# Optimization experiments

Hardware: AMD Instinct MI355X
Metric: run time of the kernel (lower is better)

## Reference

```python
import jax, jax.numpy as jnp
import numpy as np

N_PROBLEMS = 20000
N_SKILLS = 1000
EMB_SIZE = 128
TIME_LOG = 5.0
B, L = 64, 1024


def setup_inputs() -> dict:
    key = jax.random.key(0)
    ks = jax.random.split(key, 10)
    skills = jax.random.randint(ks[0], (B, L), 0, N_SKILLS)
    problems = jax.random.randint(ks[1], (B, L), 0, N_PROBLEMS)
    labels = jax.random.randint(ks[2], (B, L), 0, 2)
    times = jnp.sort(jax.random.randint(ks[3], (B, L), 0, 1_000_000), axis=-1)
    inp = jnp.stack([skills, problems, labels, times], axis=1)  # [B,4,L]
    std = 0.01
    return {
        "input": inp,
        "problem_base": std * jax.random.normal(ks[4], (N_PROBLEMS, 1), jnp.float32),
        "skill_base": std * jax.random.normal(ks[5], (N_SKILLS, 1), jnp.float32),
        "alpha_inter": std * jax.random.normal(ks[6], (N_SKILLS * 2, EMB_SIZE), jnp.float32),
        "alpha_skill": std * jax.random.normal(ks[7], (N_SKILLS, EMB_SIZE), jnp.float32),
        "beta_inter": std * jax.random.normal(ks[8], (N_SKILLS * 2, EMB_SIZE), jnp.float32),
        "beta_skill": std * jax.random.normal(ks[9], (N_SKILLS, EMB_SIZE), jnp.float32),
    }


def reference(input, problem_base, skill_base, alpha_inter, alpha_skill, beta_inter, beta_skill):
    skills = input[:, 0]    # [B,L]
    problems = input[:, 1]
    labels = input[:, 2]
    times = input[:, 3]

    mask_labels = labels * (labels < 2).astype(labels.dtype)
    inters = skills + mask_labels * N_SKILLS  # [B,L] in [0, 2*N_SKILLS)

    # pairwise Hawkes excitation / decay scores: [B,L,L]
    alphas = jnp.einsum('bie,bje->bij', alpha_inter[inters], alpha_skill[skills])
    betas = jnp.einsum('bie,bje->bij', beta_inter[inters], beta_skill[skills])
    betas = jnp.clip(betas + 1.0, 0.0, 10.0)

    dt = jnp.abs(times[:, :, None] - times[:, None, :]).astype(jnp.float32)
    log_dt = jnp.log(dt + 1e-10) / np.log(TIME_LOG)

    cross_effects = alphas * jnp.exp(-betas * log_dt)

    seq_len = skills.shape[1]
    # keep strictly-upper-triangular entries (source i before target j)
    keep = jnp.triu(jnp.ones((seq_len, seq_len), dtype=bool), k=1)
    sum_t = jnp.where(keep[None], cross_effects, 0.0).sum(axis=-2)  # [B,L]

    problem_bias = problem_base[problems][..., 0]
    skill_bias = skill_base[skills][..., 0]
    return jax.nn.sigmoid(problem_bias + skill_bias + sum_t)
```

## Files before the change

### kernel.cpp

```cpp
#include <hip/hip_runtime.h>
#include <hip/hip_bf16.h>

#define NB   64
#define SL   1024
#define EMB  128
#define NSK  1000
#define TI   64
#define NS   2

#define AI_OFF 0
#define BI_OFF 256000
#define AS_OFF 512000
#define BS_OFF 640000
#define TB_ELEMS 768000
#define ACC_BYTE_OFF (TB_ELEMS * 2)

#define AI_B 0
#define BI_B 512000
#define AS_B 1024000
#define BS_B 1280000

using short8  = __attribute__((ext_vector_type(8))) short;
using floatx4 = __attribute__((ext_vector_type(4))) float;

#define INV_LOG2_5 0.43067655807339306f

__device__ inline unsigned cvt2(float x, float y) {
    float2 f; f.x = x; f.y = y;
    __hip_bfloat162 h = __float22bfloat162_rn(f);
    unsigned u; __builtin_memcpy(&u, &h, sizeof(u));
    return u;
}

extern "C" __global__ __launch_bounds__(256)
void cvt_tables(const float* __restrict__ ai, const float* __restrict__ bi,
                const float* __restrict__ as, const float* __restrict__ bs,
                unsigned short* __restrict__ dst)
{
    const int t = blockIdx.x * 256 + threadIdx.x;
    const long e = (long)t * 8;
    const float* src;
    if      (e < 256000) src = ai + e;
    else if (e < 512000) src = bi + (e - 256000);
    else if (e < 640000) src = as + (e - 512000);
    else                 src = bs + (e - 640000);
    float4 f0 = *(const float4*)src;
    float4 f1 = *(const float4*)(src + 4);
    uint4 pk;
    pk.x = cvt2(f0.x, f0.y); pk.y = cvt2(f0.z, f0.w);
    pk.z = cvt2(f1.x, f1.y); pk.w = cvt2(f1.z, f1.w);
    *(uint4*)(dst + e) = pk;
}

__device__ float fixup_pair(const float* __restrict__ air,
                            const float* __restrict__ bir,
                            const float* __restrict__ asr,
                            const float* __restrict__ bsr) {
    float da = 0.f, db = 0.f;
#pragma unroll 8
    for (int k = 0; k < EMB; k += 4) {
        float4 a  = *(const float4*)(air + k);
        float4 s  = *(const float4*)(asr + k);
        float4 bq = *(const float4*)(bir + k);
        float4 tt = *(const float4*)(bsr + k);
        da += a.x * s.x + a.y * s.y + a.z * s.z + a.w * s.w;
        db += bq.x * tt.x + bq.y * tt.y + bq.z * tt.z + bq.w * tt.w;
    }
    float beta = fminf(fmaxf(db + 1.f, 0.f), 10.f);
    return da * __expf(beta * 14.30676558073393f);
}

extern "C" __global__ __launch_bounds__(256, 2)
void hawkes_main(const int*   __restrict__ inp,
                 const unsigned short* __restrict__ tb,
                 float*       __restrict__ acc)
{
    __shared__ uint4 ldsq[2048];
    char* ldsc = (char*)ldsq;

    const int bid  = blockIdx.x;
    const int b    = bid & (NB - 1);
    const int r    = bid >> 6;
    const int jt   = 15 - (r >> 1);
    const int s    = r & 1;
    const int tid  = threadIdx.x;
    const int w    = tid >> 6;
    const int l    = tid & 63;
    const int quad = l >> 4;
    const int col  = l & 15;
    const int wrow = w * 16;

    const int* __restrict__ binp = inp + b * 4 * SL;
    const char* __restrict__ tbc = (const char*)tb;

    const int jbase = jt * TI;

    int tjv[4];
#pragma unroll
    for (int strip = 0; strip < 4; ++strip)
        tjv[strip] = binp[3 * SL + jbase + strip * 16 + col];

    {
        const int row  = tid >> 2;
        const int sq   = tid & 3;
        const int skj  = binp[jbase + row];
        const char* srcA = tbc + AS_B + (long)skj * 256 + sq * 64;
        const char* srcB = tbc + BS_B + (long)skj * 256 + sq * 64;
        uint4 qa[4], qb[4];
#pragma unroll
        for (int u = 0; u < 4; ++u) {
            qa[u] = *(const uint4*)(srcA + u * 16);
            qb[u] = *(const uint4*)(srcB + u * 16);
        }
        const int rx = (row & 15) << 4;
        const int wb = row * 256;
#pragma unroll
        for (int u = 0; u < 4; ++u) {
            const int slot = (((4 * sq + u) << 4) ^ rx);
            *(uint4*)(ldsc + wb + slot)         = qa[u];
            *(uint4*)(ldsc + 16384 + wb + slot) = qb[u];
        }
    }
    __syncthreads();

    short8 bfa[4][4], bfb[4][4];
#pragma unroll
    for (int strip = 0; strip < 4; ++strip) {
        const int row   = strip * 16 + col;
        const int rbase = row * 256;
        const int rx    = (row & 15) << 4;
#pragma unroll
        for (int ks = 0; ks < 4; ++ks) {
            const int cb = ((quad + ks * 4) << 4) ^ rx;
            bfa[strip][ks] = *(const short8*)(ldsc + rbase + cb);
            bfb[strip][ks] = *(const short8*)(ldsc + 16384 + rbase + cb);
        }
    }

    int intrv[8];
#pragma unroll
    for (int tt = 0; tt < 8; ++tt) {
        const int arow = (s + 2 * tt) * TI + wrow + col;
        intrv[tt] = binp[arow] + binp[2 * SL + arow] * NSK;
    }

    float sum[4] = {0.f, 0.f, 0.f, 0.f};

#pragma unroll 1
    for (int it = s; it <= jt; it += NS) {
        const int tt = (it - s) >> 1;
        const long ab = (long)intrv[tt] * 256 + quad * 16;
        const char* pA = tbc + AI_B + ab;
        const char* pB = tbc + BI_B + ab;
        short8 av[4], bv[4];
#pragma unroll
        for (int ks = 0; ks < 4; ++ks) {
            av[ks] = *(const short8*)(pA + ks * 64);
            bv[ks] = *(const short8*)(pB + ks * 64);
        }
        const int4 t4 = *(const int4*)(binp + 3 * SL + it * TI + wrow + quad * 4);

        floatx4 aa[4], bb[4];
#pragma unroll
        for (int strip = 0; strip < 4; ++strip) {
            aa[strip] = floatx4{0.f, 0.f, 0.f, 0.f};
            bb[strip] = floatx4{1.f, 1.f, 1.f, 1.f};
        }
#pragma unroll
        for (int ks = 0; ks < 4; ++ks) {
#pragma unroll
            for (int strip = 0; strip < 4; ++strip) {
                aa[strip] = __builtin_amdgcn_mfma_f32_16x16x32_bf16(av[ks], bfa[strip][ks], aa[strip], 0, 0, 0);
                bb[strip] = __builtin_amdgcn_mfma_f32_16x16x32_bf16(bv[ks], bfb[strip][ks], bb[strip], 0, 0, 0);
            }
        }

#pragma unroll
        for (int strip = 0; strip < 4; ++strip) {
            const int tjs = tjv[strip];
#pragma unroll
            for (int rr = 0; rr < 4; ++rr) {
                const int ti = (rr == 0) ? t4.x : (rr == 1) ? t4.y : (rr == 2) ? t4.z : t4.w;
                const int dt = tjs - ti;
                float lc  = __log2f((float)dt);
                float nb  = fminf(fmaxf(bb[strip][rr], 0.f), 10.f) * (-INV_LOG2_5);
                float arg = (dt > 0) ? nb * lc : -__builtin_inff();
                sum[strip] += aa[strip][rr] * __builtin_amdgcn_exp2f(arg);
            }
        }
    }

#pragma unroll
    for (int strip = 0; strip < 4; ++strip) {
        sum[strip] += __shfl_xor(sum[strip], 16, 64);
        sum[strip] += __shfl_xor(sum[strip], 32, 64);
    }
    __syncthreads();
    float* red = (float*)ldsc;
    red[w * 64 + quad * 16 + col] = sum[quad];
    __syncthreads();
    if (w == 0) {
        const float tot = red[l] + red[64 + l] + red[128 + l] + red[192 + l];
        acc[(((long)s * NB + b) << 10) + jbase + l] = tot;
    }
}

extern "C" __global__ __launch_bounds__(256)
void hawkes_finalize(const int* __restrict__ inp, const float* __restrict__ pbase,
                     const float* __restrict__ sbase,
                     const float* __restrict__ ai, const float* __restrict__ as,
                     const float* __restrict__ bi, const float* __restrict__ bs,
                     const float* __restrict__ acc, float* __restrict__ out)
{
    const int t = blockIdx.x * 256 + threadIdx.x;
    const int b = t >> 10, j = t & (SL - 1);
    const int* binp = inp + b * 4 * SL;
    const int tj   = binp[3 * SL + j];
    const int sk_j = binp[j];

    float corr = 0.f;
    for (int i = j - 1; i >= 0 && binp[3 * SL + i] == tj; --i) {
        const int ski = binp[i], li = binp[2 * SL + i];
        const long intr = ski + (long)li * NSK;
        corr += fixup_pair(ai + intr * EMB, bi + intr * EMB,
                           as + (long)sk_j * EMB, bs + (long)sk_j * EMB);
    }

    float sum = acc[t] + acc[NB * SL + t] + corr;
    const float x = pbase[binp[SL + j]] + sbase[sk_j] + sum;
    out[t] = 1.f / (1.f + __expf(-x));
}

extern "C" void kernel_launch(void* const* d_in, const int* in_sizes, int n_in,
                              void* d_out, int out_size, void* d_ws, size_t ws_size,
                              hipStream_t stream) {
    const int*   inp = (const int*)d_in[0];
    const float* pb  = (const float*)d_in[1];
    const float* sb  = (const float*)d_in[2];
    const float* ai  = (const float*)d_in[3];
    const float* as  = (const float*)d_in[4];
    const float* bi  = (const float*)d_in[5];
    const float* bs  = (const float*)d_in[6];

    unsigned short* tb  = (unsigned short*)d_ws;
    float*          acc = (float*)((char*)d_ws + ACC_BYTE_OFF);

    cvt_tables<<<dim3(96000 / 256), dim3(256), 0, stream>>>(ai, bi, as, bs, tb);
    hawkes_main<<<dim3(NB * 16 * NS), dim3(256), 0, stream>>>(inp, tb, acc);
    hawkes_finalize<<<dim3(NB * SL / 256), dim3(256), 0, stream>>>(
        inp, pb, sb, ai, as, bi, bs, acc, (float*)d_out);
}
```

Measured before the change: 119.2 us.

## Stage A-operand rows through double-buffered LDS with register prefetch

Before this change, each wave gathered its alpha/beta interaction rows directly from global memory with strided per-lane loads inside the loop. Now each thread loads contiguous 64-byte chunks of the next-next tile into registers and writes them into a swizzled, double-buffered LDS region while the current tile is computed. MFMA A operands are then read from LDS. This hides gather latency and coalesces global loads. The cost is doubled LDS (64 KB per block, which may limit occupancy to 2 blocks per CU), more registers for the prefetch stage, and a block-wide barrier each iteration.

New measurement: 116.4 us. 1.02x faster.

```diff
diff --git a/kernel.cpp b/kernel.cpp
--- a/kernel.cpp
+++ b/kernel.cpp
@@ -8,10 +8,6 @@
 #define TI   64
 #define NS   2
 
-#define AI_OFF 0
-#define BI_OFF 256000
-#define AS_OFF 512000
-#define BS_OFF 640000
 #define TB_ELEMS 768000
 #define ACC_BYTE_OFF (TB_ELEMS * 2)
 
@@ -70,12 +66,39 @@
     return da * __expf(beta * 14.30676558073393f);
 }
 
+struct Stage2 { uint4 a0, a1, a2, a3, b0, b1, b2, b3; };
+
+__device__ __forceinline__ Stage2 stage_load2(const char* __restrict__ tbc,
+                                              int intr, int sq)
+{
+    const long ab = (long)intr * 256 + sq * 64;
+    const char* pA = tbc + AI_B + ab;
+    const char* pB = tbc + BI_B + ab;
+    Stage2 s;
+    s.a0 = *(const uint4*)(pA);      s.a1 = *(const uint4*)(pA + 16);
+    s.a2 = *(const uint4*)(pA + 32); s.a3 = *(const uint4*)(pA + 48);
+    s.b0 = *(const uint4*)(pB);      s.b1 = *(const uint4*)(pB + 16);
+    s.b2 = *(const uint4*)(pB + 32); s.b3 = *(const uint4*)(pB + 48);
+    return s;
+}
+
+__device__ __forceinline__ void stage_write2(char* buf, int srow, int wslot,
+                                             const Stage2& s)
+{
+    char* pA = buf + srow * 256 + wslot;
+    char* pAx = buf + srow * 256 + (wslot ^ 16);
+    *(uint4*)(pA)        = s.a0;  *(uint4*)(pA + 128)  = s.a1;
+    *(uint4*)(pAx)       = s.a2;  *(uint4*)(pAx + 128) = s.a3;
+    *(uint4*)(pA + 16384)  = s.b0;  *(uint4*)(pA + 16384 + 128)  = s.b1;
+    *(uint4*)(pAx + 16384) = s.b2;  *(uint4*)(pAx + 16384 + 128) = s.b3;
+}
+
 extern "C" __global__ __launch_bounds__(256, 2)
 void hawkes_main(const int*   __restrict__ inp,
                  const unsigned short* __restrict__ tb,
                  float*       __restrict__ acc)
 {
-    __shared__ uint4 ldsq[2048];
+    __shared__ uint4 ldsq[4096];
     char* ldsc = (char*)ldsq;
 
     const int bid  = blockIdx.x;
@@ -92,7 +115,6 @@
 
     const int* __restrict__ binp = inp + b * 4 * SL;
     const char* __restrict__ tbc = (const char*)tb;
-
     const int jbase = jt * TI;
 
     int tjv[4];
@@ -137,55 +159,78 @@
         }
     }
 
+    const int srow  = tid >> 2;
+    const int sq    = tid & 3;
+    const int wslot = (((2 * sq) ^ (srow & 7)) << 4);
     int intrv[8];
 #pragma unroll
     for (int tt = 0; tt < 8; ++tt) {
-        const int arow = (s + 2 * tt) * TI + wrow + col;
+        const int arow = (s + 2 * tt) * TI + srow;
         intrv[tt] = binp[arow] + binp[2 * SL + arow] * NSK;
     }
 
+    int roff[4];
+    {
+        const int qh = quad >> 1, ql = quad & 1, c7 = col & 7;
+#pragma unroll
+        for (int ks = 0; ks < 4; ++ks)
+            roff[ks] = (wrow + col) * 256 + ql * 128 + (((2 * ks + qh) ^ c7) << 4);
+    }
+
     float sum[4] = {0.f, 0.f, 0.f, 0.f};
 
+    if (s <= jt) {
+        const int nt = ((jt - s) >> 1) + 1;
+
+        Stage2 rS = stage_load2(tbc, intrv[0], sq);
+        __syncthreads();
+        stage_write2(ldsc, srow, wslot, rS);
+        if (nt > 1) rS = stage_load2(tbc, intrv[1], sq);
+
 #pragma unroll 1
-    for (int it = s; it <= jt; it += NS) {
-        const int tt = (it - s) >> 1;
-        const long ab = (long)intrv[tt] * 256 + quad * 16;
-        const char* pA = tbc + AI_B + ab;
-        const char* pB = tbc + BI_B + ab;
-        short8 av[4], bv[4];
-#pragma unroll
-        for (int ks = 0; ks < 4; ++ks) {
-            av[ks] = *(const short8*)(pA + ks * 64);
-            bv[ks] = *(const short8*)(pB + ks * 64);
-        }
-        const int4 t4 = *(const int4*)(binp + 3 * SL + it * TI + wrow + quad * 4);
-
-        floatx4 aa[4], bb[4];
-#pragma unroll
-        for (int strip = 0; strip < 4; ++strip) {
-            aa[strip] = floatx4{0.f, 0.f, 0.f, 0.f};
-            bb[strip] = floatx4{1.f, 1.f, 1.f, 1.f};
-        }
-#pragma unroll
-        for (int ks = 0; ks < 4; ++ks) {
+        for (int t = 0; t < nt; ++t) {
+            __syncthreads();
+            const int cur = (t & 1) << 15;
+            if (t + 1 < nt) stage_write2(ldsc + (cur ^ 32768), srow, wslot, rS);
+            if (t + 2 < nt) rS = stage_load2(tbc, intrv[t + 2], sq);
+
+            const int it = s + 2 * t;
+            const char* bufA = ldsc + cur;
+            short8 av[4], bv[4];
+#pragma unroll
+            for (int ks = 0; ks < 4; ++ks) {
+                av[ks] = *(const short8*)(bufA + roff[ks]);
+                bv[ks] = *(const short8*)(bufA + 16384 + roff[ks]);
+            }
+            const int4 t4 = *(const int4*)(binp + 3 * SL + it * TI + wrow + quad * 4);
+
+            floatx4 aa[4], bb[4];
 #pragma unroll
             for (int strip = 0; strip < 4; ++strip) {
-                aa[strip] = __builtin_amdgcn_mfma_f32_16x16x32_bf16(av[ks], bfa[strip][ks], aa[strip], 0, 0, 0);
-                bb[strip] = __builtin_amdgcn_mfma_f32_16x16x32_bf16(bv[ks], bfb[strip][ks], bb[strip], 0, 0, 0);
-            }
-        }
-
-#pragma unroll
-        for (int strip = 0; strip < 4; ++strip) {
-            const int tjs = tjv[strip];
-#pragma unroll
-            for (int rr = 0; rr < 4; ++rr) {
-                const int ti = (rr == 0) ? t4.x : (rr == 1) ? t4.y : (rr == 2) ? t4.z : t4.w;
-                const int dt = tjs - ti;
-                float lc  = __log2f((float)dt);
-                float nb  = fminf(fmaxf(bb[strip][rr], 0.f), 10.f) * (-INV_LOG2_5);
-                float arg = (dt > 0) ? nb * lc : -__builtin_inff();
-                sum[strip] += aa[strip][rr] * __builtin_amdgcn_exp2f(arg);
+                aa[strip] = floatx4{0.f, 0.f, 0.f, 0.f};
+                bb[strip] = floatx4{1.f, 1.f, 1.f, 1.f};
+            }
+#pragma unroll
+            for (int ks = 0; ks < 4; ++ks) {
+#pragma unroll
+                for (int strip = 0; strip < 4; ++strip) {
+                    aa[strip] = __builtin_amdgcn_mfma_f32_16x16x32_bf16(av[ks], bfa[strip][ks], aa[strip], 0, 0, 0);
+                    bb[strip] = __builtin_amdgcn_mfma_f32_16x16x32_bf16(bv[ks], bfb[strip][ks], bb[strip], 0, 0, 0);
+                }
+            }
+
+#pragma unroll
+            for (int strip = 0; strip < 4; ++strip) {
+                const int tjs = tjv[strip];
+#pragma unroll
+                for (int rr = 0; rr < 4; ++rr) {
+                    const int ti = (rr == 0) ? t4.x : (rr == 1) ? t4.y : (rr == 2) ? t4.z : t4.w;
+                    const int dt = tjs - ti;
+                    float lc  = __log2f((float)dt);
+                    float nb  = fminf(fmaxf(bb[strip][rr], 0.f), 10.f) * (-INV_LOG2_5);
+                    float arg = (dt > 0) ? nb * lc : -__builtin_inff();
+                    sum[strip] += aa[strip][rr] * __builtin_amdgcn_exp2f(arg);
+                }
             }
         }
     }
```
